# Kernel optimization log

Measured on AMD Instinct MI355X. Metric: run time of the kernel, lower is better.

## Reference

```python
import jax, jax.numpy as jnp
import numpy as np

EPS = 1e-6
K_HOPS = 2  # SGConv K


def setup_inputs() -> dict:
    key = jax.random.key(0)
    k1, k2, k3, k4 = jax.random.split(key, 4)
    B, Kk, C, T = 32, 8, 64, 250
    E, H = 4096, 128
    x = jax.random.normal(k1, (B, Kk, C, T), dtype=jnp.float32)
    edge_index = jax.random.randint(k2, (2, E), 0, C, dtype=jnp.int64)
    edge_weights = jax.random.uniform(k3, (E,), dtype=jnp.float32)
    W = jax.random.normal(k4, (H, Kk * T), dtype=jnp.float32) * 0.02
    b = jnp.zeros((H,), dtype=jnp.float32)
    return {"x": x, "edge_index": edge_index, "edge_weights": edge_weights, "W": W, "b": b}


def reference(x, edge_index, edge_weights, W, b):
    B, Kk, C, T = x.shape
    N = C  # nodes
    x = x.reshape(B, N, Kk * T)  # (B, N, F)

    # clamp non-positive edge weights to epsilon (mirrors in-place .data clamp)
    w = jnp.where(edge_weights <= 0, EPS, edge_weights)

    # gcn_norm with self loops (fill value 1.0)
    src, dst = edge_index[0], edge_index[1]
    loop = jnp.arange(N, dtype=edge_index.dtype)
    src = jnp.concatenate([src, loop])
    dst = jnp.concatenate([dst, loop])
    w = jnp.concatenate([w, jnp.ones((N,), w.dtype)])
    deg = jnp.zeros((N,), w.dtype).at[dst].add(w)
    dinv = jnp.where(deg > 0, deg ** -0.5, jnp.zeros_like(deg))
    norm = dinv[src] * w * dinv[dst]  # (E+N,)

    # K hops of gather -> weight -> scatter-add aggregation
    for _ in range(K_HOPS):
        msg = x[:, src, :] * norm[None, :, None]        # (B, E+N, F)
        x = jnp.zeros_like(x).at[:, dst, :].add(msg)    # (B, N, F)

    # final linear: y = x @ W^T + b
    return jnp.einsum('bnf,hf->bnh', x, W) + b
```

## Files before the change

kernel.cpp:

```cpp
#include <hip/hip_runtime.h>
#include <hip/hip_bf16.h>

#define EPSW 1e-6f

typedef __attribute__((ext_vector_type(4))) float floatx4;
typedef __attribute__((ext_vector_type(4))) unsigned int uintx4;
typedef __attribute__((ext_vector_type(8))) short shortx8;

__device__ __forceinline__ unsigned short f2bf(float f) {
    unsigned int u = __float_as_uint(f);
    u = (u + 0x7fffu + ((u >> 16) & 1u)) >> 16;
    return (unsigned short)u;
}

__device__ __forceinline__ unsigned int pk2(float lo, float hi) {
    return (unsigned int)f2bf(lo) | ((unsigned int)f2bf(hi) << 16);
}

__device__ __forceinline__ uintx4 pk8(floatx4 a, floatx4 b) {
    uintx4 r;
    r.x = pk2(a.x, a.y); r.y = pk2(a.z, a.w);
    r.z = pk2(b.x, b.y); r.w = pk2(b.z, b.w);
    return r;
}

__global__ __launch_bounds__(512) void gemm_mt(
        const float* __restrict__ x,
        const float* __restrict__ W,
        const int* __restrict__ ei,
        const float* __restrict__ ew,
        float* __restrict__ zp,
        float* __restrict__ Mt) {
    __shared__ __align__(16) unsigned char smem[2][24576];
    const int bid = blockIdx.x;
    const int t   = threadIdx.x;

    if (bid < 4) {
        float* A    = (float*)smem;
        float* deg  = A + 4096;
        float* dinv = deg + 64;
        if (t < 64) deg[t] = 1.0f;
        for (int i = t; i < 4096; i += 512) A[i] = 0.0f;
        __syncthreads();
        const int* srcp = ei;
        const int* dstp = ei + 4096;
#pragma unroll
        for (int i = 0; i < 8; ++i) {
            const int e = i * 512 + t;
            float w = ew[e];
            w = (w <= 0.0f) ? EPSW : w;
            atomicAdd(&deg[dstp[e]], w);
        }
        __syncthreads();
        if (t < 64) dinv[t] = 1.0f / sqrtf(deg[t]);
        __syncthreads();
#pragma unroll
        for (int i = 0; i < 8; ++i) {
            const int e = i * 512 + t;
            float w = ew[e];
            w = (w <= 0.0f) ? EPSW : w;
            const int s = srcp[e], d = dstp[e];
            atomicAdd(&A[d * 64 + s], dinv[s] * w * dinv[d]);
        }
        if (t < 64) atomicAdd(&A[t * 64 + t], dinv[t] * dinv[t]);
        __syncthreads();
        const int c  = t & 63;
        const int n0 = bid * 16 + (t >> 6);
        const int n1 = n0 + 8;
        float s0 = 0.0f, s1 = 0.0f;
#pragma unroll 8
        for (int k = 0; k < 64; ++k) {
            const float akc = A[k * 64 + c];
            s0 += A[n0 * 64 + k] * akc;
            s1 += A[n1 * 64 + k] * akc;
        }
        Mt[c * 64 + n0] = s0;
        Mt[c * 64 + n1] = s1;
        return;
    }

    const int g     = bid - 4;
    const int ks    = g >> 5;
    const int bb    = g & 31;
    const int rbase = bb * 64;
    const int kbase = ks * 256;

    const int wave = t >> 6, lane = t & 63;
    const int m = lane & 15, q = lane >> 4;
    const int kq = t & 7;
    const int rw = t >> 3;

    floatx4 acc[4];
#pragma unroll
    for (int rt = 0; rt < 4; ++rt) acc[rt] = (floatx4){0.f, 0.f, 0.f, 0.f};

    floatx4 va0, va1, wb00, wb01, wb10, wb11;

#define LOADC(c)                                                              \
    {                                                                         \
        const int k_ = kbase + (c) * 64 + kq * 8;                             \
        if (k_ < 2000) {                                                      \
            const float* pa_ = x + (size_t)(rbase + rw) * 2000 + k_;          \
            const float* p0_ = W + (size_t)rw * 2000 + k_;                    \
            const float* p1_ = W + (size_t)(rw + 64) * 2000 + k_;             \
            va0  = *(const floatx4*)pa_;  va1  = *(const floatx4*)(pa_ + 4);  \
            wb00 = *(const floatx4*)p0_;  wb01 = *(const floatx4*)(p0_ + 4);  \
            wb10 = *(const floatx4*)p1_;  wb11 = *(const floatx4*)(p1_ + 4);  \
        } else {                                                              \
            va0 = va1 = wb00 = wb01 = wb10 = wb11 =                           \
                (floatx4){0.f, 0.f, 0.f, 0.f};                                \
        }                                                                     \
    }

#define WRITEC(c)                                                             \
    {                                                                         \
        unsigned char* sb_ = smem[(c) & 1];                                   \
        *(uintx4*)(sb_ + kq * 1024 + rw * 16)               = pk8(va0, va1);  \
        *(uintx4*)(sb_ + 8192 + kq * 2048 + rw * 16)        = pk8(wb00, wb01);\
        *(uintx4*)(sb_ + 8192 + kq * 2048 + (rw + 64) * 16) = pk8(wb10, wb11);\
    }

    LOADC(0);
    for (int c = 0; c < 4; ++c) {
        WRITEC(c);
        if (c < 3) LOADC(c + 1);
        __syncthreads();
        const unsigned char* sb = smem[c & 1];
#pragma unroll
        for (int p = 0; p < 2; ++p) {
            const int kgq = p * 4 + q;
            shortx8 a[4];
#pragma unroll
            for (int rt = 0; rt < 4; ++rt)
                a[rt] = *(const shortx8*)(sb + kgq * 1024 + (rt * 16 + m) * 16);
            const shortx8 bf = *(const shortx8*)(sb + 8192 + kgq * 2048 +
                                                 (wave * 16 + m) * 16);
#pragma unroll
            for (int rt = 0; rt < 4; ++rt)
                acc[rt] = __builtin_amdgcn_mfma_f32_16x16x32_bf16(
                    a[rt], bf, acc[rt], 0, 0, 0);
        }
        __syncthreads();
    }
#undef LOADC
#undef WRITEC

    float* zslice = zp + ((size_t)ks * 2048 + rbase) * 128;
    const int h = wave * 16 + m;
#pragma unroll
    for (int rt = 0; rt < 4; ++rt) {
#pragma unroll
        for (int v = 0; v < 4; ++v) {
            const int n = rt * 16 + q * 4 + v;
            zslice[n * 128 + h] = acc[rt][v];
        }
    }
}

__global__ __launch_bounds__(256) void apply_M(const float* __restrict__ zp,
                                               const float* __restrict__ Mtg,
                                               const float* __restrict__ bias,
                                               float* __restrict__ y) {
    __shared__ float Ms[4096];
    __shared__ float zs[64][16];
    const int b  = blockIdx.x;
    const int hc = blockIdx.y;
    const int t  = threadIdx.x;
#pragma unroll
    for (int i = 0; i < 16; ++i) Ms[i * 256 + t] = Mtg[i * 256 + t];
#pragma unroll
    for (int i = 0; i < 4; ++i) {
        const int idx = i * 256 + t;
        const int mr = idx >> 4, hh = idx & 15;
        float s = 0.0f;
#pragma unroll
        for (int ks = 0; ks < 8; ++ks)
            s += zp[((size_t)ks * 2048 + b * 64 + mr) * 128 + hc * 16 + hh];
        zs[mr][hh] = s;
    }
    __syncthreads();
    const int h  = t & 15;
    const int n0 = (t >> 4) * 4;
    const float bv = bias[hc * 16 + h];
    float s0 = bv, s1 = bv, s2 = bv, s3 = bv;
#pragma unroll
    for (int mm = 0; mm < 64; ++mm) {
        const float zv = zs[mm][h];
        s0 += Ms[mm * 64 + n0 + 0] * zv;
        s1 += Ms[mm * 64 + n0 + 1] * zv;
        s2 += Ms[mm * 64 + n0 + 2] * zv;
        s3 += Ms[mm * 64 + n0 + 3] * zv;
    }
    float* yp = y + (size_t)b * 8192 + (size_t)n0 * 128 + hc * 16 + h;
    yp[0]   = s0;
    yp[128] = s1;
    yp[256] = s2;
    yp[384] = s3;
}

extern "C" void kernel_launch(void* const* d_in, const int* in_sizes, int n_in,
                              void* d_out, int out_size, void* d_ws, size_t ws_size,
                              hipStream_t stream) {
    const float* x    = (const float*)d_in[0];
    const int*   ei   = (const int*)d_in[1];
    const float* ew   = (const float*)d_in[2];
    const float* W    = (const float*)d_in[3];
    const float* bias = (const float*)d_in[4];
    float* y = (float*)d_out;

    float* zp = (float*)d_ws;
    float* Mt = zp + 2097152;

    gemm_mt<<<260, 512, 0, stream>>>(x, W, ei, ew, zp, Mt);
    apply_M<<<dim3(32, 8), 256, 0, stream>>>(zp, Mt, bias, y);
}
```

Before: 88.61 us.

## Split GEMM into smaller 32-row blocks with two-deep register prefetch

Halves the GEMM tile from 64 to 32 rows and uses 256-thread blocks, doubling the grid to 516 blocks so more CUs are busy. Each wave now computes a 2x2 MFMA tile over two column groups. Global loads are prefetched two chunks ahead into double register buffers, and the trailing barrier after each chunk is removed. The adjacency/M blocks move to the end of the grid and each computes 16 rows with 256 threads. Risks: more register pressure and duplicated W loads across the extra blocks. Dropping the second barrier may also allow a race on the double-buffered shared memory, since chunk c+2's write can overlap with reads of chunk c.

```diff
diff --git a/kernel.cpp b/kernel.cpp
--- a/kernel.cpp
+++ b/kernel.cpp
@@ -24,29 +24,30 @@
     return r;
 }
 
-__global__ __launch_bounds__(512) void gemm_mt(
+__global__ __launch_bounds__(256) void gemm_mt(
         const float* __restrict__ x,
         const float* __restrict__ W,
         const int* __restrict__ ei,
         const float* __restrict__ ew,
         float* __restrict__ zp,
         float* __restrict__ Mt) {
-    __shared__ __align__(16) unsigned char smem[2][24576];
+    __shared__ __align__(16) unsigned char smem[2][20480];
     const int bid = blockIdx.x;
     const int t   = threadIdx.x;
 
-    if (bid < 4) {
+    if (bid >= 512) {
+        const int bm = bid - 512;
         float* A    = (float*)smem;
         float* deg  = A + 4096;
         float* dinv = deg + 64;
         if (t < 64) deg[t] = 1.0f;
-        for (int i = t; i < 4096; i += 512) A[i] = 0.0f;
+        for (int i = t; i < 4096; i += 256) A[i] = 0.0f;
         __syncthreads();
         const int* srcp = ei;
         const int* dstp = ei + 4096;
 #pragma unroll
-        for (int i = 0; i < 8; ++i) {
-            const int e = i * 512 + t;
+        for (int i = 0; i < 16; ++i) {
+            const int e = i * 256 + t;
             float w = ew[e];
             w = (w <= 0.0f) ? EPSW : w;
             atomicAdd(&deg[dstp[e]], w);
@@ -55,8 +56,8 @@
         if (t < 64) dinv[t] = 1.0f / sqrtf(deg[t]);
         __syncthreads();
 #pragma unroll
-        for (int i = 0; i < 8; ++i) {
-            const int e = i * 512 + t;
+        for (int i = 0; i < 16; ++i) {
+            const int e = i * 256 + t;
             float w = ew[e];
             w = (w <= 0.0f) ? EPSW : w;
             const int s = srcp[e], d = dstp[e];
@@ -65,24 +66,25 @@
         if (t < 64) atomicAdd(&A[t * 64 + t], dinv[t] * dinv[t]);
         __syncthreads();
         const int c  = t & 63;
-        const int n0 = bid * 16 + (t >> 6);
-        const int n1 = n0 + 8;
-        float s0 = 0.0f, s1 = 0.0f;
+        const int rr = t >> 6;
+        float s0 = 0.f, s1 = 0.f, s2 = 0.f, s3 = 0.f;
 #pragma unroll 8
         for (int k = 0; k < 64; ++k) {
             const float akc = A[k * 64 + c];
-            s0 += A[n0 * 64 + k] * akc;
-            s1 += A[n1 * 64 + k] * akc;
-        }
-        Mt[c * 64 + n0] = s0;
-        Mt[c * 64 + n1] = s1;
+            const float* an = A + (bm * 16 + rr * 4) * 64 + k;
+            s0 += an[0]   * akc;
+            s1 += an[64]  * akc;
+            s2 += an[128] * akc;
+            s3 += an[192] * akc;
+        }
+        float* mo = Mt + c * 64 + bm * 16 + rr * 4;
+        mo[0] = s0; mo[1] = s1; mo[2] = s2; mo[3] = s3;
         return;
     }
 
-    const int g     = bid - 4;
-    const int ks    = g >> 5;
-    const int bb    = g & 31;
-    const int rbase = bb * 64;
+    const int ks    = bid & 7;
+    const int bb2   = bid >> 3;
+    const int rbase = bb2 * 32;
     const int kbase = ks * 256;
 
     const int wave = t >> 6, lane = t & 63;
@@ -90,71 +92,92 @@
     const int kq = t & 7;
     const int rw = t >> 3;
 
-    floatx4 acc[4];
-#pragma unroll
-    for (int rt = 0; rt < 4; ++rt) acc[rt] = (floatx4){0.f, 0.f, 0.f, 0.f};
-
-    floatx4 va0, va1, wb00, wb01, wb10, wb11;
+    floatx4 acc[2][2];
+#pragma unroll
+    for (int rt = 0; rt < 2; ++rt)
+#pragma unroll
+        for (int hh = 0; hh < 2; ++hh)
+            acc[rt][hh] = (floatx4){0.f, 0.f, 0.f, 0.f};
+
+    floatx4 rA[2][2];
+    floatx4 rB[2][8];
 
 #define LOADC(c)                                                              \
     {                                                                         \
+        const int s_ = (c) & 1;                                               \
         const int k_ = kbase + (c) * 64 + kq * 8;                             \
         if (k_ < 2000) {                                                      \
             const float* pa_ = x + (size_t)(rbase + rw) * 2000 + k_;          \
-            const float* p0_ = W + (size_t)rw * 2000 + k_;                    \
-            const float* p1_ = W + (size_t)(rw + 64) * 2000 + k_;             \
-            va0  = *(const floatx4*)pa_;  va1  = *(const floatx4*)(pa_ + 4);  \
-            wb00 = *(const floatx4*)p0_;  wb01 = *(const floatx4*)(p0_ + 4);  \
-            wb10 = *(const floatx4*)p1_;  wb11 = *(const floatx4*)(p1_ + 4);  \
+            rA[s_][0] = *(const floatx4*)pa_;                                 \
+            rA[s_][1] = *(const floatx4*)(pa_ + 4);                           \
+            _Pragma("unroll")                                                 \
+            for (int j_ = 0; j_ < 4; ++j_) {                                  \
+                const float* pw_ = W + (size_t)(rw + 32 * j_) * 2000 + k_;    \
+                rB[s_][j_ * 2]     = *(const floatx4*)pw_;                    \
+                rB[s_][j_ * 2 + 1] = *(const floatx4*)(pw_ + 4);              \
+            }                                                                 \
         } else {                                                              \
-            va0 = va1 = wb00 = wb01 = wb10 = wb11 =                           \
-                (floatx4){0.f, 0.f, 0.f, 0.f};                                \
+            rA[s_][0] = rA[s_][1] = (floatx4){0.f, 0.f, 0.f, 0.f};            \
+            _Pragma("unroll")                                                 \
+            for (int j_ = 0; j_ < 8; ++j_)                                    \
+                rB[s_][j_] = (floatx4){0.f, 0.f, 0.f, 0.f};                   \
         }                                                                     \
     }
 
 #define WRITEC(c)                                                             \
     {                                                                         \
-        unsigned char* sb_ = smem[(c) & 1];                                   \
-        *(uintx4*)(sb_ + kq * 1024 + rw * 16)               = pk8(va0, va1);  \
-        *(uintx4*)(sb_ + 8192 + kq * 2048 + rw * 16)        = pk8(wb00, wb01);\
-        *(uintx4*)(sb_ + 8192 + kq * 2048 + (rw + 64) * 16) = pk8(wb10, wb11);\
+        const int s_ = (c) & 1;                                               \
+        unsigned char* sb_ = smem[s_];                                        \
+        *(uintx4*)(sb_ + kq * 512 + rw * 16) = pk8(rA[s_][0], rA[s_][1]);     \
+        _Pragma("unroll")                                                     \
+        for (int j_ = 0; j_ < 4; ++j_)                                        \
+            *(uintx4*)(sb_ + 4096 + kq * 2048 + (rw + 32 * j_) * 16) =        \
+                pk8(rB[s_][j_ * 2], rB[s_][j_ * 2 + 1]);                      \
     }
 
     LOADC(0);
+    LOADC(1);
+#pragma unroll
     for (int c = 0; c < 4; ++c) {
         WRITEC(c);
-        if (c < 3) LOADC(c + 1);
+        if (c < 2) LOADC(c + 2);
         __syncthreads();
         const unsigned char* sb = smem[c & 1];
 #pragma unroll
         for (int p = 0; p < 2; ++p) {
             const int kgq = p * 4 + q;
-            shortx8 a[4];
-#pragma unroll
-            for (int rt = 0; rt < 4; ++rt)
-                a[rt] = *(const shortx8*)(sb + kgq * 1024 + (rt * 16 + m) * 16);
-            const shortx8 bf = *(const shortx8*)(sb + 8192 + kgq * 2048 +
-                                                 (wave * 16 + m) * 16);
-#pragma unroll
-            for (int rt = 0; rt < 4; ++rt)
-                acc[rt] = __builtin_amdgcn_mfma_f32_16x16x32_bf16(
-                    a[rt], bf, acc[rt], 0, 0, 0);
-        }
-        __syncthreads();
+            shortx8 af[2];
+#pragma unroll
+            for (int rt = 0; rt < 2; ++rt)
+                af[rt] = *(const shortx8*)(sb + kgq * 512 + (rt * 16 + m) * 16);
+            shortx8 bf[2];
+#pragma unroll
+            for (int hh = 0; hh < 2; ++hh)
+                bf[hh] = *(const shortx8*)(sb + 4096 + kgq * 2048 +
+                                           ((wave + hh * 4) * 16 + m) * 16);
+#pragma unroll
+            for (int rt = 0; rt < 2; ++rt)
+#pragma unroll
+                for (int hh = 0; hh < 2; ++hh)
+                    acc[rt][hh] = __builtin_amdgcn_mfma_f32_16x16x32_bf16(
+                        af[rt], bf[hh], acc[rt][hh], 0, 0, 0);
+        }
     }
 #undef LOADC
 #undef WRITEC
 
     float* zslice = zp + ((size_t)ks * 2048 + rbase) * 128;
-    const int h = wave * 16 + m;
-#pragma unroll
-    for (int rt = 0; rt < 4; ++rt) {
-#pragma unroll
-        for (int v = 0; v < 4; ++v) {
-            const int n = rt * 16 + q * 4 + v;
-            zslice[n * 128 + h] = acc[rt][v];
-        }
-    }
+#pragma unroll
+    for (int rt = 0; rt < 2; ++rt)
+#pragma unroll
+        for (int hh = 0; hh < 2; ++hh) {
+            const int h = (wave + hh * 4) * 16 + m;
+#pragma unroll
+            for (int v = 0; v < 4; ++v) {
+                const int n = rt * 16 + q * 4 + v;
+                zslice[n * 128 + h] = acc[rt][hh][v];
+            }
+        }
 }
 
 __global__ __launch_bounds__(256) void apply_M(const float* __restrict__ zp,
@@ -211,6 +234,6 @@
     float* zp = (float*)d_ws;
     float* Mt = zp + 2097152;
 
-    gemm_mt<<<260, 512, 0, stream>>>(x, W, ei, ew, zp, Mt);
+    gemm_mt<<<516, 256, 0, stream>>>(x, W, ei, ew, zp, Mt);
     apply_M<<<dim3(32, 8), 256, 0, stream>>>(zp, Mt, bias, y);
 }
```

Result: slower. 93.57 us (+5.6%).

## Preload full W K-slice into LDS and double-buffer X with deeper prefetch

Applied to the files above, without the earlier changes.

The GEMM blocks now convert and stage the whole 128x256 W slice for their K split into a single LDS buffer up front. Only X tiles stream through a two-slot buffer, prefetched two chunks ahead in registers, which removes the trailing barrier per chunk. The block-to-tile mapping is reordered so the K split varies fastest, and the four graph-matrix blocks move to the end of the grid. LDS use grows to 80KB per block, which limits how many blocks can share a CU. W is also loaded all at once before any compute, so that load is not overlapped with MFMA work.

```diff
diff --git a/kernel.cpp b/kernel.cpp
--- a/kernel.cpp
+++ b/kernel.cpp
@@ -31,11 +31,12 @@
         const float* __restrict__ ew,
         float* __restrict__ zp,
         float* __restrict__ Mt) {
-    __shared__ __align__(16) unsigned char smem[2][24576];
+    __shared__ __align__(16) unsigned char smem[81920];
     const int bid = blockIdx.x;
     const int t   = threadIdx.x;
 
-    if (bid < 4) {
+    if (bid >= 256) {
+        const int bm = bid - 256;
         float* A    = (float*)smem;
         float* deg  = A + 4096;
         float* dinv = deg + 64;
@@ -65,7 +66,7 @@
         if (t < 64) atomicAdd(&A[t * 64 + t], dinv[t] * dinv[t]);
         __syncthreads();
         const int c  = t & 63;
-        const int n0 = bid * 16 + (t >> 6);
+        const int n0 = bm * 16 + (t >> 6);
         const int n1 = n0 + 8;
         float s0 = 0.0f, s1 = 0.0f;
 #pragma unroll 8
@@ -79,11 +80,27 @@
         return;
     }
 
-    const int g     = bid - 4;
-    const int ks    = g >> 5;
-    const int bb    = g & 31;
-    const int rbase = bb * 64;
+    const int ks    = bid & 7;
+    const int rt2   = bid >> 3;
+    const int rbase = rt2 * 64;
     const int kbase = ks * 256;
+
+    unsigned char* Wl = smem;
+    unsigned char* Xl = smem + 65536;
+
+#pragma unroll
+    for (int i = 0; i < 8; ++i) {
+        const int G  = i * 512 + t;
+        const int kg = G >> 7, h = G & 127;
+        const int k  = kbase + kg * 8;
+        floatx4 v0 = (floatx4){0.f, 0.f, 0.f, 0.f};
+        floatx4 v1 = (floatx4){0.f, 0.f, 0.f, 0.f};
+        if (k < 2000) {
+            v0 = *(const floatx4*)(W + (size_t)h * 2000 + k);
+            v1 = *(const floatx4*)(W + (size_t)h * 2000 + k + 4);
+        }
+        *(uintx4*)(Wl + ((size_t)(kg * 128 + h)) * 16) = pk8(v0, v1);
+    }
 
     const int wave = t >> 6, lane = t & 63;
     const int m = lane & 15, q = lane >> 4;
@@ -94,56 +111,53 @@
 #pragma unroll
     for (int rt = 0; rt < 4; ++rt) acc[rt] = (floatx4){0.f, 0.f, 0.f, 0.f};
 
-    floatx4 va0, va1, wb00, wb01, wb10, wb11;
-
-#define LOADC(c)                                                              \
+    floatx4 rX[2][2];
+
+#define LOADX(c)                                                              \
     {                                                                         \
+        const int s_ = (c) & 1;                                               \
         const int k_ = kbase + (c) * 64 + kq * 8;                             \
         if (k_ < 2000) {                                                      \
-            const float* pa_ = x + (size_t)(rbase + rw) * 2000 + k_;          \
-            const float* p0_ = W + (size_t)rw * 2000 + k_;                    \
-            const float* p1_ = W + (size_t)(rw + 64) * 2000 + k_;             \
-            va0  = *(const floatx4*)pa_;  va1  = *(const floatx4*)(pa_ + 4);  \
-            wb00 = *(const floatx4*)p0_;  wb01 = *(const floatx4*)(p0_ + 4);  \
-            wb10 = *(const floatx4*)p1_;  wb11 = *(const floatx4*)(p1_ + 4);  \
+            const float* p_ = x + (size_t)(rbase + rw) * 2000 + k_;           \
+            rX[s_][0] = *(const floatx4*)p_;                                  \
+            rX[s_][1] = *(const floatx4*)(p_ + 4);                            \
         } else {                                                              \
-            va0 = va1 = wb00 = wb01 = wb10 = wb11 =                           \
-                (floatx4){0.f, 0.f, 0.f, 0.f};                                \
+            rX[s_][0] = rX[s_][1] = (floatx4){0.f, 0.f, 0.f, 0.f};            \
         }                                                                     \
     }
 
-#define WRITEC(c)                                                             \
+#define WRITEX(c)                                                             \
     {                                                                         \
-        unsigned char* sb_ = smem[(c) & 1];                                   \
-        *(uintx4*)(sb_ + kq * 1024 + rw * 16)               = pk8(va0, va1);  \
-        *(uintx4*)(sb_ + 8192 + kq * 2048 + rw * 16)        = pk8(wb00, wb01);\
-        *(uintx4*)(sb_ + 8192 + kq * 2048 + (rw + 64) * 16) = pk8(wb10, wb11);\
-    }
-
-    LOADC(0);
+        const int s_ = (c) & 1;                                               \
+        *(uintx4*)(Xl + s_ * 8192 + (kq * 64 + rw) * 16) =                    \
+            pk8(rX[s_][0], rX[s_][1]);                                        \
+    }
+
+    LOADX(0);
+    LOADX(1);
+#pragma unroll
     for (int c = 0; c < 4; ++c) {
-        WRITEC(c);
-        if (c < 3) LOADC(c + 1);
-        __syncthreads();
-        const unsigned char* sb = smem[c & 1];
+        WRITEX(c);
+        if (c < 2) LOADX(c + 2);
+        __syncthreads();
+        const unsigned char* sx = Xl + (c & 1) * 8192;
 #pragma unroll
         for (int p = 0; p < 2; ++p) {
             const int kgq = p * 4 + q;
-            shortx8 a[4];
+            shortx8 af[4];
 #pragma unroll
             for (int rt = 0; rt < 4; ++rt)
-                a[rt] = *(const shortx8*)(sb + kgq * 1024 + (rt * 16 + m) * 16);
-            const shortx8 bf = *(const shortx8*)(sb + 8192 + kgq * 2048 +
-                                                 (wave * 16 + m) * 16);
+                af[rt] = *(const shortx8*)(sx + (kgq * 64 + rt * 16 + m) * 16);
+            const shortx8 bf = *(const shortx8*)(
+                Wl + (((c * 8 + kgq) * 128) + wave * 16 + m) * 16);
 #pragma unroll
             for (int rt = 0; rt < 4; ++rt)
                 acc[rt] = __builtin_amdgcn_mfma_f32_16x16x32_bf16(
-                    a[rt], bf, acc[rt], 0, 0, 0);
-        }
-        __syncthreads();
-    }
-#undef LOADC
-#undef WRITEC
+                    af[rt], bf, acc[rt], 0, 0, 0);
+        }
+    }
+#undef LOADX
+#undef WRITEX
 
     float* zslice = zp + ((size_t)ks * 2048 + rbase) * 128;
     const int h = wave * 16 + m;
```

New measurement: 89.26 us. No clear change (+0.7%).

## Prefetch all K chunks upfront, drop trailing barrier, reorder block mapping

Applied to the files above, without the earlier changes.

The GEMM blocks now issue global loads for all four K chunks into registers before any compute, instead of loading one chunk ahead. The second __syncthreads per iteration is removed, which is safe because the double-buffered LDS is protected by the next iteration's barrier. The M-computing blocks move to the end of the grid, and k-slice and row-tile indices are remapped so adjacent blocks share x rows. This exposes more memory-level parallelism and cuts barrier stalls, at the cost of more registers per thread.

```diff
diff --git a/kernel.cpp b/kernel.cpp
--- a/kernel.cpp
+++ b/kernel.cpp
@@ -35,7 +35,8 @@
     const int bid = blockIdx.x;
     const int t   = threadIdx.x;
 
-    if (bid < 4) {
+    if (bid >= 256) {
+        const int bm = bid - 256;
         float* A    = (float*)smem;
         float* deg  = A + 4096;
         float* dinv = deg + 64;
@@ -65,7 +66,7 @@
         if (t < 64) atomicAdd(&A[t * 64 + t], dinv[t] * dinv[t]);
         __syncthreads();
         const int c  = t & 63;
-        const int n0 = bid * 16 + (t >> 6);
+        const int n0 = bm * 16 + (t >> 6);
         const int n1 = n0 + 8;
         float s0 = 0.0f, s1 = 0.0f;
 #pragma unroll 8
@@ -79,10 +80,9 @@
         return;
     }
 
-    const int g     = bid - 4;
-    const int ks    = g >> 5;
-    const int bb    = g & 31;
-    const int rbase = bb * 64;
+    const int ks    = bid & 7;
+    const int rt2   = bid >> 3;
+    const int rbase = rt2 * 64;
     const int kbase = ks * 256;
 
     const int wave = t >> 6, lane = t & 63;
@@ -94,7 +94,8 @@
 #pragma unroll
     for (int rt = 0; rt < 4; ++rt) acc[rt] = (floatx4){0.f, 0.f, 0.f, 0.f};
 
-    floatx4 va0, va1, wb00, wb01, wb10, wb11;
+    floatx4 sA[4][2];
+    floatx4 sB[4][4];
 
 #define LOADC(c)                                                              \
     {                                                                         \
@@ -103,11 +104,15 @@
             const float* pa_ = x + (size_t)(rbase + rw) * 2000 + k_;          \
             const float* p0_ = W + (size_t)rw * 2000 + k_;                    \
             const float* p1_ = W + (size_t)(rw + 64) * 2000 + k_;             \
-            va0  = *(const floatx4*)pa_;  va1  = *(const floatx4*)(pa_ + 4);  \
-            wb00 = *(const floatx4*)p0_;  wb01 = *(const floatx4*)(p0_ + 4);  \
-            wb10 = *(const floatx4*)p1_;  wb11 = *(const floatx4*)(p1_ + 4);  \
+            sA[c][0] = *(const floatx4*)pa_;                                  \
+            sA[c][1] = *(const floatx4*)(pa_ + 4);                            \
+            sB[c][0] = *(const floatx4*)p0_;                                  \
+            sB[c][1] = *(const floatx4*)(p0_ + 4);                            \
+            sB[c][2] = *(const floatx4*)p1_;                                  \
+            sB[c][3] = *(const floatx4*)(p1_ + 4);                            \
         } else {                                                              \
-            va0 = va1 = wb00 = wb01 = wb10 = wb11 =                           \
+            sA[c][0] = sA[c][1] = (floatx4){0.f, 0.f, 0.f, 0.f};              \
+            sB[c][0] = sB[c][1] = sB[c][2] = sB[c][3] =                       \
                 (floatx4){0.f, 0.f, 0.f, 0.f};                                \
         }                                                                     \
     }
@@ -115,32 +120,38 @@
 #define WRITEC(c)                                                             \
     {                                                                         \
         unsigned char* sb_ = smem[(c) & 1];                                   \
-        *(uintx4*)(sb_ + kq * 1024 + rw * 16)               = pk8(va0, va1);  \
-        *(uintx4*)(sb_ + 8192 + kq * 2048 + rw * 16)        = pk8(wb00, wb01);\
-        *(uintx4*)(sb_ + 8192 + kq * 2048 + (rw + 64) * 16) = pk8(wb10, wb11);\
+        *(uintx4*)(sb_ + kq * 1024 + rw * 16)               =                 \
+            pk8(sA[c][0], sA[c][1]);                                          \
+        *(uintx4*)(sb_ + 8192 + kq * 2048 + rw * 16)        =                 \
+            pk8(sB[c][0], sB[c][1]);                                          \
+        *(uintx4*)(sb_ + 8192 + kq * 2048 + (rw + 64) * 16) =                 \
+            pk8(sB[c][2], sB[c][3]);                                          \
     }
 
     LOADC(0);
+    LOADC(1);
+    LOADC(2);
+    LOADC(3);
+
+#pragma unroll
     for (int c = 0; c < 4; ++c) {
         WRITEC(c);
-        if (c < 3) LOADC(c + 1);
         __syncthreads();
         const unsigned char* sb = smem[c & 1];
 #pragma unroll
         for (int p = 0; p < 2; ++p) {
             const int kgq = p * 4 + q;
-            shortx8 a[4];
+            shortx8 af[4];
 #pragma unroll
             for (int rt = 0; rt < 4; ++rt)
-                a[rt] = *(const shortx8*)(sb + kgq * 1024 + (rt * 16 + m) * 16);
+                af[rt] = *(const shortx8*)(sb + kgq * 1024 + (rt * 16 + m) * 16);
             const shortx8 bf = *(const shortx8*)(sb + 8192 + kgq * 2048 +
                                                  (wave * 16 + m) * 16);
 #pragma unroll
             for (int rt = 0; rt < 4; ++rt)
                 acc[rt] = __builtin_amdgcn_mfma_f32_16x16x32_bf16(
-                    a[rt], bf, acc[rt], 0, 0, 0);
-        }
-        __syncthreads();
+                    af[rt], bf, acc[rt], 0, 0, 0);
+        }
     }
 #undef LOADC
 #undef WRITEC
```

Measured after the change: 89.89 us. No clear change (+1.4%).
